# Kernel tuning notes

Hardware: AMD Instinct MI355X
Metric: run time of the kernel (lower is better)

The kernel has to match this reference:

```python
import jax, jax.numpy as jnp
import numpy as np


def conv(x, w, b=None, stride=1, pad=0):
    out = jax.lax.conv_general_dilated(x, w, (stride, stride), [(pad, pad), (pad, pad)],
                                       dimension_numbers=('NCHW', 'OIHW', 'NCHW'))
    if b is not None:
        out = out + b[None, :, None, None]
    return out


def fsm(x, att_w, conv_w):
    # FeatureSelectionModule: global-avg-pool -> 1x1 conv -> sigmoid gate, residual, 1x1 proj
    gap = jnp.mean(x, axis=(2, 3), keepdims=True)
    atten = jax.nn.sigmoid(conv(gap, att_w))
    return conv(x + x * atten, conv_w)


def mdcn(x, offset, mask, weight, bias, pad=1, G=8):
    # Modulated deformable conv v2: stride 1, dilation 1, conv groups 1, G deformable groups.
    N, C, H, W = x.shape
    Co, Ci, kh, kw = weight.shape
    K = kh * kw
    Cg = C // G
    off = offset.reshape(N, G, 2, K, H, W)          # per-group (y, x) offsets per kernel tap
    msk = mask.reshape(N, G, 1, K, H, W)
    ky, kx = jnp.meshgrid(jnp.arange(kh), jnp.arange(kw), indexing='ij')
    py = (jnp.arange(H, dtype=x.dtype)[None, None, None, :, None] - pad) + ky.reshape(1, 1, K, 1, 1) + off[:, :, 0]
    px = (jnp.arange(W, dtype=x.dtype)[None, None, None, None, :] - pad) + kx.reshape(1, 1, K, 1, 1) + off[:, :, 1]
    y0 = jnp.floor(py)
    x0 = jnp.floor(px)
    wy1 = py - y0
    wy0 = 1.0 - wy1
    wx1 = px - x0
    wx0 = 1.0 - wx1
    xg = x.reshape(N, G, Cg, H * W)

    def gather(iy, ix):
        valid = (iy >= 0) & (iy <= H - 1) & (ix >= 0) & (ix <= W - 1)
        idx = (jnp.clip(iy, 0, H - 1) * W + jnp.clip(ix, 0, W - 1)).astype(jnp.int32)
        v = jnp.take_along_axis(xg, idx.reshape(N, G, 1, K * H * W), axis=3)
        return v.reshape(N, G, Cg, K, H, W) * valid[:, :, None].astype(x.dtype)

    val = ((wy0 * wx0)[:, :, None] * gather(y0, x0)
         + (wy0 * wx1)[:, :, None] * gather(y0, x0 + 1)
         + (wy1 * wx0)[:, :, None] * gather(y0 + 1, x0)
         + (wy1 * wx1)[:, :, None] * gather(y0 + 1, x0 + 1))
    val = val * msk                                   # [N,G,Cg,K,H,W]
    out = jnp.einsum('ngckhw,ogck->nohw', val, weight.reshape(Co, G, Cg, K))
    return out + bias[None, :, None, None]


def align(feat_l, feat_s, att_w, fsm_w, off_w, om_w, om_b, dcn_w, dcn_b):
    # FeatureAlign_V2
    N, Cs, H, W = feat_s.shape[0], feat_s.shape[1], feat_l.shape[2], feat_l.shape[3]
    feat_up = jax.image.resize(feat_s, (N, Cs, H, W), 'bilinear')  # align_corners=False
    feat_arm = fsm(feat_l, att_w, fsm_w)
    off_feat = conv(jnp.concatenate([feat_arm, feat_up * 2.0], axis=1), off_w)
    om = conv(off_feat, om_w, om_b, pad=1)            # conv_offset_mask: 3*G*K channels
    o1, o2, mk = jnp.split(om, 3, axis=1)
    offset = jnp.concatenate([o1, o2], axis=1)
    mask = jax.nn.sigmoid(mk)
    feat_align = jax.nn.relu(mdcn(feat_up, offset, mask, dcn_w, dcn_b))
    return feat_align + feat_arm


def setup_inputs() -> dict:
    key = jax.random.key(0)
    ks = iter(jax.random.split(key, 64))

    def w(shape):
        fan_in = shape[1] * shape[2] * shape[3]
        return jax.random.normal(next(ks), shape, jnp.float32) / np.float32(np.sqrt(fan_in))

    def b(n):
        return jnp.zeros((n,), jnp.float32)

    d = {}
    d['c2'] = jax.random.normal(next(ks), (1, 256, 128, 128), jnp.float32)
    d['c3'] = jax.random.normal(next(ks), (1, 512, 64, 64), jnp.float32)
    d['c4'] = jax.random.normal(next(ks), (1, 1024, 32, 32), jnp.float32)
    d['c5'] = jax.random.normal(next(ks), (1, 2048, 16, 16), jnp.float32)
    OC = 256
    OM = 8 * 3 * 9  # deformable_groups * (2 offsets + 1 mask) * k*k = 216
    for tag, in_nc in (('16', 1024), ('8', 512), ('4', 256)):
        d['att_w' + tag] = w((in_nc, in_nc, 1, 1))
        d['fsm_w' + tag] = w((OC, in_nc, 1, 1))
        d['off_w' + tag] = w((OC, 2 * OC, 1, 1))
        d['om_w' + tag] = w((OM, OC, 3, 3))
        d['om_b' + tag] = b(OM)
        d['dcn_w' + tag] = w((OC, OC, 3, 3))
        d['dcn_b' + tag] = b(OC)
        d['out_w' + tag] = w((OC, OC, 3, 3))
        d['out_b' + tag] = b(OC)
    d['lat_w'] = w((OC, 2048, 1, 1))
    d['lat_b'] = b(OC)
    return d


def reference(c2, c3, c4, c5,
              att_w16, fsm_w16, off_w16, om_w16, om_b16, dcn_w16, dcn_b16, out_w16, out_b16,
              att_w8, fsm_w8, off_w8, om_w8, om_b8, dcn_w8, dcn_b8, out_w8, out_b8,
              att_w4, fsm_w4, off_w4, om_w4, om_b4, dcn_w4, dcn_b4, out_w4, out_b4,
              lat_w, lat_b):
    # top-down pass, coarsest first (matches FAN.forward with reversed inputs)
    p5 = conv(c5, lat_w, lat_b)
    f16 = align(c4, p5, att_w16, fsm_w16, off_w16, om_w16, om_b16, dcn_w16, dcn_b16)
    p4 = conv(f16, out_w16, out_b16, pad=1)
    f8 = align(c3, f16, att_w8, fsm_w8, off_w8, om_w8, om_b8, dcn_w8, dcn_b8)
    p3 = conv(f8, out_w8, out_b8, pad=1)
    f4 = align(c2, f8, att_w4, fsm_w4, off_w4, om_w4, om_b4, dcn_w4, dcn_b4)
    p2 = conv(f4, out_w4, out_b4, pad=1)
    return (p2, p3, p4, p5)
```

## Files before the change

kernel.cpp:

```cpp
#include <hip/hip_runtime.h>
#include <hip/hip_bf16.h>

typedef __hip_bfloat16 bf16;
typedef __attribute__((ext_vector_type(8))) short bf16x8;
typedef __attribute__((ext_vector_type(4))) float floatx4;

__device__ __forceinline__ float b2f(bf16 v) { return __bfloat162float(v); }
__device__ __forceinline__ bf16 f2b(float v) { return __float2bfloat16(v); }
__device__ __forceinline__ float us2f(unsigned short u) {
  union { unsigned int i; float f; } v; v.i = ((unsigned int)u) << 16; return v.f;
}
__device__ __forceinline__ unsigned short f2us(float f) {
  bf16 h = f2b(f); return *(unsigned short*)&h;
}

__global__ __launch_bounds__(256) void gap_kernel(const float* __restrict__ x,
                                                  float* __restrict__ gap,
                                                  int HW, float inv) {
  int c = blockIdx.x;
  const float* p = x + (size_t)c * HW;
  float s = 0.f;
  for (int i = threadIdx.x; i < HW; i += 256) s += p[i];
  __shared__ float red[256];
  red[threadIdx.x] = s;
  __syncthreads();
  for (int w = 128; w > 0; w >>= 1) {
    if (threadIdx.x < w) red[threadIdx.x] += red[threadIdx.x + w];
    __syncthreads();
  }
  if (threadIdx.x == 0) gap[c] = red[0] * inv;
}

__global__ __launch_bounds__(256) void atten_kernel(const float* __restrict__ w,
                                                    const float* __restrict__ gap,
                                                    float* __restrict__ scale, int Ci) {
  int wave = threadIdx.x >> 6, lane = threadIdx.x & 63;
  int o = blockIdx.x * 4 + wave;
  const float4* wr = (const float4*)(w + (size_t)o * Ci);
  const float4* g4 = (const float4*)gap;
  int n4 = Ci >> 2;
  float s = 0.f;
  for (int i = lane; i < n4; i += 64) {
    float4 a = wr[i], b = g4[i];
    s += a.x * b.x + a.y * b.y + a.z * b.z + a.w * b.w;
  }
#pragma unroll
  for (int off = 32; off > 0; off >>= 1) s += __shfl_down(s, off);
  if (lane == 0) scale[o] = 1.f + 1.f / (1.f + expf(-s));
}

__global__ __launch_bounds__(256) void upsample2x_nhwc_kernel(
    const bf16* __restrict__ src, bf16* __restrict__ dst, int Hs, int Ws) {
  int p = blockIdx.x;
  int c = threadIdx.x;
  int W = Ws * 2;
  int y = p / W, x = p - y * W;
  float fy = y * 0.5f - 0.25f;
  float fx = x * 0.5f - 0.25f;
  int y0 = (int)floorf(fy), x0 = (int)floorf(fx);
  float wy1 = fy - (float)y0, wx1 = fx - (float)x0;
  int y0c = min(max(y0, 0), Hs - 1);
  int y1c = min(max(y0 + 1, 0), Hs - 1);
  int x0c = min(max(x0, 0), Ws - 1);
  int x1c = min(max(x0 + 1, 0), Ws - 1);
  float v00 = b2f(src[(size_t)(y0c * Ws + x0c) * 256 + c]);
  float v01 = b2f(src[(size_t)(y0c * Ws + x1c) * 256 + c]);
  float v10 = b2f(src[(size_t)(y1c * Ws + x0c) * 256 + c]);
  float v11 = b2f(src[(size_t)(y1c * Ws + x1c) * 256 + c]);
  float v = (1.f - wy1) * ((1.f - wx1) * v00 + wx1 * v01)
          + wy1 * ((1.f - wx1) * v10 + wx1 * v11);
  dst[(size_t)p * 256 + c] = f2b(v);
}

__global__ __launch_bounds__(256) void packw1_kernel(const float* __restrict__ w,
                                                     bf16* __restrict__ BP, int K) {
  int idx = blockIdx.x * 256 + threadIdx.x;
  int j = idx & 7;
  int o = (idx >> 3) & 255;
  int kc8 = idx >> 11;
  int k = kc8 * 8 + j;
  BP[idx] = f2b(w[(size_t)o * K + k]);
}

__global__ __launch_bounds__(256) void pack_level_kernel(
    const float* __restrict__ fsm_w, int Ci,
    const float* __restrict__ off_w, const float* __restrict__ om_w,
    const float* __restrict__ dcn_w, const float* __restrict__ out_w,
    bf16* __restrict__ BPfsm, bf16* __restrict__ BPoff, bf16* __restrict__ BPom,
    bf16* __restrict__ BPdcn, bf16* __restrict__ BPout) {
  int b = blockIdx.x;
  if (b < Ci) {
    int idx = b * 256 + threadIdx.x;
    int j = idx & 7, o = (idx >> 3) & 255, k = (idx >> 11) * 8 + j;
    BPfsm[idx] = f2b(fsm_w[(size_t)o * Ci + k]);
    return;
  }
  b -= Ci;
  if (b < 512) {
    int idx = b * 256 + threadIdx.x;
    int j = idx & 7, o = (idx >> 3) & 255, k = (idx >> 11) * 8 + j;
    BPoff[idx] = f2b(off_w[(size_t)o * 512 + k]);
    return;
  }
  b -= 512;
  const float* w;
  bf16* BP;
  int Co;
  if (b < 2304) { w = om_w; BP = BPom; Co = 216; }
  else if (b < 4608) {
    int idx = (b - 2304) * 256 + threadIdx.x;
    int j = idx & 7, o = (idx >> 3) & 255;
    int k = (idx >> 11) * 8 + j;
    int tap = k >> 8, ci = k & 255;
    BPdcn[idx] = f2b(dcn_w[((size_t)o * 256 + ci) * 9 + tap]);
    return;
  } else { w = out_w; BP = BPout; Co = 256; b -= 2304; }
  int idx = (b % 2304) * 256 + threadIdx.x;
  int j = idx & 7;
  int t1 = idx >> 3;
  int o = t1 & 255;
  int t2 = t1 >> 8;
  int q = t2 & 3;
  int t3 = t2 >> 2;
  int tap = t3 % 9;
  int c = t3 / 9;
  int ci = c * 32 + q * 8 + j;
  float v = (o < Co) ? w[((size_t)o * 256 + ci) * 9 + tap] : 0.f;
  BP[idx] = f2b(v);
}

template <bool NCHW1, typename TA1>
__global__ __launch_bounds__(256) void conv1x1_mfma_kernel(
    const TA1* __restrict__ A1, const float* __restrict__ scaleA,
    const bf16* __restrict__ A2, float scaleB,
    int Ci1, int Ci2, int HW,
    const bf16* __restrict__ BP, const float* __restrict__ bias,
    float* __restrict__ out1, bf16* __restrict__ out2, int ns2) {
  __shared__ __align__(16) bf16 sA[1024];
  int p0 = blockIdx.x * 32;
  int tid = threadIdx.x;
  int pix = tid & 31, sub = tid >> 5;
  int pix2 = tid >> 3, sub8 = tid & 7;
  int lane = tid & 63, wave = tid >> 6;
  int pg = wave & 1, cg = wave >> 1;
  int q = lane >> 4, n = lane & 15;

  floatx4 acc[4];
#pragma unroll
  for (int nt = 0; nt < 4; ++nt) acc[nt] = (floatx4)0.f;

  int nch = (Ci1 + Ci2) >> 5;
  for (int kc = 0; kc < nch; ++kc) {
    int ci0 = kc << 5;
    if (NCHW1 && ci0 < Ci1) {
#pragma unroll
      for (int it = 0; it < 4; ++it) {
        int cil = it * 8 + sub;
        float x = (float)A1[(size_t)(ci0 + cil) * HW + p0 + pix];
        if (scaleA) x *= scaleA[ci0 + cil];
        sA[((cil >> 3) * 32 + pix) * 8 + (cil & 7)] = f2b(x);
      }
    } else {
      const bf16* src; int cb; bool scl;
      if (!NCHW1 && ci0 < Ci1) {
        src = (const bf16*)(const void*)A1; cb = ci0; scl = false;
      } else {
        src = A2; cb = ci0 - Ci1; scl = true;
      }
      ushort4 raw = *(const ushort4*)&src[(size_t)(p0 + pix2) * 256 + cb + sub8 * 4];
      if (scl) {
        raw.x = f2us(us2f(raw.x) * scaleB);
        raw.y = f2us(us2f(raw.y) * scaleB);
        raw.z = f2us(us2f(raw.z) * scaleB);
        raw.w = f2us(us2f(raw.w) * scaleB);
      }
      *(ushort4*)&sA[((sub8 >> 1) * 32 + pix2) * 8 + (sub8 & 1) * 4] = raw;
    }
    __syncthreads();
    bf16x8 a = *(const bf16x8*)&sA[(q * 32 + pg * 16 + n) * 8];
    const bf16* bp = BP + ((size_t)(kc * 4 + q) * 256 + blockIdx.y * 128 + cg * 64) * 8;
#pragma unroll
    for (int nt = 0; nt < 4; ++nt) {
      bf16x8 b = *(const bf16x8*)&bp[(nt * 16 + n) * 8];
      acc[nt] = __builtin_amdgcn_mfma_f32_16x16x32_bf16(a, b, acc[nt], 0, 0, 0);
    }
    __syncthreads();
  }

  int pbase = p0 + pg * 16 + q * 4;
#pragma unroll
  for (int nt = 0; nt < 4; ++nt) {
    int o = blockIdx.y * 128 + cg * 64 + nt * 16 + n;
    float bv = bias ? bias[o] : 0.f;
#pragma unroll
    for (int r = 0; r < 4; ++r) {
      float v = acc[nt][r] + bv;
      if (out1) out1[(size_t)o * HW + pbase + r] = v;
      if (out2) out2[(size_t)(pbase + r) * ns2 + o] = f2b(v);
    }
  }
}

__global__ __launch_bounds__(256) void conv1x1_part_kernel(
    const float* __restrict__ A1, int HW,
    const bf16* __restrict__ BP, float* __restrict__ PART) {
  __shared__ __align__(16) bf16 sA[1024];
  int p0 = blockIdx.x * 32;
  int tid = threadIdx.x;
  int pix = tid & 31, sub = tid >> 5;
  int lane = tid & 63, wave = tid >> 6;
  int pg = wave & 1, cg = wave >> 1;
  int q = lane >> 4, n = lane & 15;

  floatx4 acc[4];
#pragma unroll
  for (int nt = 0; nt < 4; ++nt) acc[nt] = (floatx4)0.f;

  int kc0 = blockIdx.z * 8;
  for (int kcl = 0; kcl < 8; ++kcl) {
    int kc = kc0 + kcl;
    int ci0 = kc << 5;
#pragma unroll
    for (int it = 0; it < 4; ++it) {
      int cil = it * 8 + sub;
      sA[((cil >> 3) * 32 + pix) * 8 + (cil & 7)] =
          f2b(A1[(size_t)(ci0 + cil) * HW + p0 + pix]);
    }
    __syncthreads();
    bf16x8 a = *(const bf16x8*)&sA[(q * 32 + pg * 16 + n) * 8];
    const bf16* bp = BP + ((size_t)(kc * 4 + q) * 256 + blockIdx.y * 128 + cg * 64) * 8;
#pragma unroll
    for (int nt = 0; nt < 4; ++nt) {
      bf16x8 b = *(const bf16x8*)&bp[(nt * 16 + n) * 8];
      acc[nt] = __builtin_amdgcn_mfma_f32_16x16x32_bf16(a, b, acc[nt], 0, 0, 0);
    }
    __syncthreads();
  }

  int pbase = p0 + pg * 16 + q * 4;
#pragma unroll
  for (int nt = 0; nt < 4; ++nt) {
    int o = blockIdx.y * 128 + cg * 64 + nt * 16 + n;
#pragma unroll
    for (int r = 0; r < 4; ++r)
      PART[((size_t)blockIdx.z * 256 + o) * HW + pbase + r] = acc[nt][r];
  }
}

__global__ __launch_bounds__(256) void reduce_p5_kernel(
    const float* __restrict__ PART, const float* __restrict__ bias,
    float* __restrict__ out1, bf16* __restrict__ out2, int HW, int KS) {
  int o = blockIdx.x;
  int p = threadIdx.x;
  float s = bias[o];
  for (int z = 0; z < KS; ++z) s += PART[((size_t)z * 256 + o) * HW + p];
  out1[(size_t)o * HW + p] = s;
  out2[(size_t)p * 256 + o] = f2b(s);
}

template <int S>
__global__ __launch_bounds__(256) void conv3x3v2_kernel(
    const bf16* __restrict__ in, const bf16* __restrict__ BP,
    const float* __restrict__ bias,
    int H, int W, int Co,
    float* __restrict__ out1, bf16* __restrict__ out2, int ns2) {
  constexpr int P = 32 * S + 2;
  constexpr int TASKS = 3 * P * 8;
  constexpr int ITS = (TASKS + 255) / 256;
  __shared__ __align__(16) bf16 sA[2][4 * 3 * P * 8];
  int HW = H * W;
  int segs = W / (32 * S);
  int y = blockIdx.x / segs;
  int x0 = (blockIdx.x - y * segs) * (32 * S);
  int tid = threadIdx.x;
  int lane = tid & 63, wave = tid >> 6;
  int pg = wave & 1, cg = wave >> 1;
  int q = lane >> 4, n = lane & 15;

  int dstIdx[ITS], srcOff[ITS];
  bool act[ITS], val[ITS];
#pragma unroll
  for (int it = 0; it < ITS; ++it) {
    int tt = it * 256 + tid;
    act[it] = (tt < TASKS);
    int sub8 = tt & 7;
    int rp = tt >> 3;
    int row = rp / P;
    int pxl = rp - row * P;
    int yy = y + row - 1;
    int xg = x0 + pxl - 1;
    bool v = act[it] && ((unsigned)yy < (unsigned)H) && ((unsigned)xg < (unsigned)W);
    val[it] = v;
    srcOff[it] = v ? ((yy * W + xg) * 256 + sub8 * 4) : 0;
    dstIdx[it] = (((sub8 >> 1) * 3 + row) * P + pxl) * 8 + (sub8 & 1) * 4;
  }

  ushort4 pv[ITS];
  auto load_regs = [&](int kc) {
    int cb = kc << 5;
#pragma unroll
    for (int it = 0; it < ITS; ++it) {
      ushort4 z = {0, 0, 0, 0};
      pv[it] = val[it] ? *(const ushort4*)&in[(size_t)srcOff[it] + cb] : z;
    }
  };
  auto store_lds = [&](int buf) {
#pragma unroll
    for (int it = 0; it < ITS; ++it)
      if (act[it]) *(ushort4*)&sA[buf][dstIdx[it]] = pv[it];
  };

  floatx4 acc[S][4];
#pragma unroll
  for (int s = 0; s < S; ++s)
#pragma unroll
    for (int nt = 0; nt < 4; ++nt) acc[s][nt] = (floatx4)0.f;

  load_regs(0);
  store_lds(0);
  __syncthreads();
  load_regs(1);

  for (int kc = 0; kc < 8; ++kc) {
    const bf16* sv = &sA[kc & 1][0];
    const bf16* bpc = BP + (size_t)kc * 73728;
#pragma unroll
    for (int tap = 0; tap < 9; ++tap) {
      int ty = tap / 3, tx = tap % 3;
      bf16x8 a[S];
#pragma unroll
      for (int s = 0; s < S; ++s)
        a[s] = *(const bf16x8*)&sv[((q * 3 + ty) * P + tx + s * 32 + pg * 16 + n) * 8];
      const bf16* bp = bpc + ((size_t)(tap * 4 + q) * 256 + blockIdx.y * 128 + cg * 64) * 8;
#pragma unroll
      for (int nt = 0; nt < 4; ++nt) {
        bf16x8 b = *(const bf16x8*)&bp[(nt * 16 + n) * 8];
#pragma unroll
        for (int s = 0; s < S; ++s)
          acc[s][nt] = __builtin_amdgcn_mfma_f32_16x16x32_bf16(a[s], b, acc[s][nt], 0, 0, 0);
      }
    }
    if (kc < 7) {
      store_lds((kc + 1) & 1);
      __syncthreads();
      if (kc < 6) load_regs(kc + 2);
    }
  }

#pragma unroll
  for (int s = 0; s < S; ++s) {
    int pbase = y * W + x0 + s * 32 + pg * 16 + q * 4;
#pragma unroll
    for (int nt = 0; nt < 4; ++nt) {
      int o = blockIdx.y * 128 + cg * 64 + nt * 16 + n;
      if (o < Co) {
        float bv = bias ? bias[o] : 0.f;
#pragma unroll
        for (int r = 0; r < 4; ++r) {
          float v = acc[s][nt][r] + bv;
          if (out1) out1[(size_t)o * HW + pbase + r] = v;
          if (out2) out2[(size_t)(pbase + r) * ns2 + o] = f2b(v);
        }
      }
    }
  }
}

__global__ __launch_bounds__(512, 4) void mdcn_mfma_kernel(
    const bf16* __restrict__ UPn, const bf16* __restrict__ OM,
    const bf16* __restrict__ BP, const float* __restrict__ dcn_b,
    const bf16* __restrict__ ARM, bf16* __restrict__ F,
    int H, int W, int wshift) {
  __shared__ __align__(16) bf16 sval[2][32 * 272];
  __shared__ float4 mw[2304];
  __shared__ int mi[2304];
  int pb = blockIdx.x * 32;
  int tid = threadIdx.x;

  for (int t2 = tid; t2 < 2304; t2 += 512) {
    int px_ = t2 & 31, g = (t2 >> 5) & 7, tap = t2 >> 8;
    int ky = tap / 3, kx = tap - ky * 3;
    int p = pb + px_;
    int y = p >> wshift, x = p & (W - 1);
    const bf16* omp = OM + (size_t)p * 216;
    float dy = b2f(omp[g * 18 + tap]);
    float dx = b2f(omp[g * 18 + 9 + tap]);
    float mm = 1.f / (1.f + expf(-b2f(omp[144 + g * 9 + tap])));
    float fpy = (float)(y - 1 + ky) + dy;
    float fpx = (float)(x - 1 + kx) + dx;
    fpy = fminf(fmaxf(fpy, -1.0e4f), 1.0e4f);
    fpx = fminf(fmaxf(fpx, -1.0e4f), 1.0e4f);
    float fy0 = floorf(fpy), fx0 = floorf(fpx);
    float wy1 = fpy - fy0, wx1 = fpx - fx0;
    float wy0 = 1.f - wy1, wx0 = 1.f - wx1;
    int iy0 = (int)fy0, ix0 = (int)fx0;
    bool vy0 = (unsigned)iy0 < (unsigned)H;
    bool vy1 = (unsigned)(iy0 + 1) < (unsigned)H;
    bool vx0 = (unsigned)ix0 < (unsigned)W;
    bool vx1 = (unsigned)(ix0 + 1) < (unsigned)W;
    float w00 = (vy0 && vx0) ? mm * wy0 * wx0 : 0.f;
    float w01 = (vy0 && vx1) ? mm * wy0 * wx1 : 0.f;
    float w10 = (vy1 && vx0) ? mm * wy1 * wx0 : 0.f;
    float w11 = (vy1 && vx1) ? mm * wy1 * wx1 : 0.f;
    int iy0c = min(max(iy0, 0), H - 1);
    int iy1c = min(max(iy0 + 1, 0), H - 1);
    int ix0c = min(max(ix0, 0), W - 1);
    int ix1c = min(max(ix0 + 1, 0), W - 1);
    mw[t2] = make_float4(w00, w01, w10, w11);
    mi[t2] = (iy0c * W + ix0c) | ((ix1c - ix0c) << 20) | ((iy1c - iy0c) << 21);
  }
  __syncthreads();

  int l4 = tid & 7;
  int px = (tid >> 3) & 31;
  int gh = tid >> 8;
  int lane = tid & 63, wave = tid >> 6;
  int q = lane >> 4, n = lane & 15;
  int rowb = l4 >> 1;
  int woff = px * 8 + (l4 & 1) * 4;

  floatx4 acc[2][2];
#pragma unroll
  for (int m = 0; m < 2; ++m)
#pragma unroll
    for (int nt = 0; nt < 2; ++nt) acc[m][nt] = (floatx4)0.f;

  ushort4 gl[4][4];
  auto gatherLoad = [&](int t) {
    int base = t * 256 + px + gh * 128;
#pragma unroll
    for (int gg = 0; gg < 4; ++gg) {
      int g = gh * 4 + gg;
      int mv = mi[base + gg * 32];
      int idx = mv & 0x3FFFF;
      int dxs = (mv >> 20) & 1;
      int dyW = ((mv >> 21) & 1) * W;
      const bf16* up = UPn + (size_t)idx * 256 + g * 32 + l4 * 4;
      gl[gg][0] = *(const ushort4*)(up);
      gl[gg][1] = *(const ushort4*)(up + dxs * 256);
      gl[gg][2] = *(const ushort4*)(up + dyW * 256);
      gl[gg][3] = *(const ushort4*)(up + (dyW + dxs) * 256);
    }
  };
  auto gatherStore = [&](int t) {
    bf16* sv = &sval[t & 1][0];
    int base = t * 256 + px + gh * 128;
#pragma unroll
    for (int gg = 0; gg < 4; ++gg) {
      int g = gh * 4 + gg;
      float4 wv = mw[base + gg * 32];
      ushort4 u00 = gl[gg][0], u01 = gl[gg][1], u10 = gl[gg][2], u11 = gl[gg][3];
      ushort4 o4;
      o4.x = f2us(wv.x * us2f(u00.x) + wv.y * us2f(u01.x)
                + wv.z * us2f(u10.x) + wv.w * us2f(u11.x));
      o4.y = f2us(wv.x * us2f(u00.y) + wv.y * us2f(u01.y)
                + wv.z * us2f(u10.y) + wv.w * us2f(u11.y));
      o4.z = f2us(wv.x * us2f(u00.z) + wv.y * us2f(u01.z)
                + wv.z * us2f(u10.z) + wv.w * us2f(u11.z));
      o4.w = f2us(wv.x * us2f(u00.w) + wv.y * us2f(u01.w)
                + wv.z * us2f(u10.w) + wv.w * us2f(u11.w));
      *(ushort4*)&sv[(g * 4 + rowb) * 272 + woff] = o4;
    }
  };

  gatherLoad(0);
  gatherStore(0);
  for (int t = 0; t < 9; ++t) {
    __syncthreads();
    if (t < 8) gatherLoad(t + 1);
    const bf16* sv = &sval[t & 1][0];
    const bf16* bpt = BP + ((size_t)(t * 32) * 256 + wave * 32) * 8;
#pragma unroll
    for (int kc = 0; kc < 8; ++kc) {
      int R = kc * 4 + q;
      bf16x8 a0 = *(const bf16x8*)&sv[R * 272 + n * 8];
      bf16x8 a1 = *(const bf16x8*)&sv[R * 272 + (16 + n) * 8];
      const bf16* bp = bpt + (size_t)R * 2048;
      bf16x8 b0 = *(const bf16x8*)&bp[n * 8];
      bf16x8 b1 = *(const bf16x8*)&bp[(16 + n) * 8];
      acc[0][0] = __builtin_amdgcn_mfma_f32_16x16x32_bf16(a0, b0, acc[0][0], 0, 0, 0);
      acc[0][1] = __builtin_amdgcn_mfma_f32_16x16x32_bf16(a0, b1, acc[0][1], 0, 0, 0);
      acc[1][0] = __builtin_amdgcn_mfma_f32_16x16x32_bf16(a1, b0, acc[1][0], 0, 0, 0);
      acc[1][1] = __builtin_amdgcn_mfma_f32_16x16x32_bf16(a1, b1, acc[1][1], 0, 0, 0);
    }
    if (t < 8) gatherStore(t + 1);
  }

#pragma unroll
  for (int m = 0; m < 2; ++m) {
#pragma unroll
    for (int nt = 0; nt < 2; ++nt) {
      int o = wave * 32 + nt * 16 + n;
      float bv = dcn_b[o];
#pragma unroll
      for (int r = 0; r < 4; ++r) {
        int p = pb + m * 16 + q * 4 + r;
        float v = fmaxf(acc[m][nt][r] + bv, 0.f) + b2f(ARM[(size_t)p * 256 + o]);
        F[(size_t)p * 256 + o] = f2b(v);
      }
    }
  }
}

extern "C" void kernel_launch(void* const* d_in, const int* in_sizes, int n_in,
                              void* d_out, int out_size, void* d_ws, size_t ws_size,
                              hipStream_t stream) {
  const float* c2 = (const float*)d_in[0];
  const float* c3 = (const float*)d_in[1];
  const float* c4 = (const float*)d_in[2];
  const float* c5 = (const float*)d_in[3];
  const float* lat_w = (const float*)d_in[31];
  const float* lat_b = (const float*)d_in[32];
  float* out = (float*)d_out;
  (void)ws_size; (void)in_sizes; (void)n_in; (void)out_size;

  const size_t p2_off = 0;
  const size_t p3_off = 4194304;
  const size_t p4_off = p3_off + 1048576;
  const size_t p5_off = p4_off + 262144;

  char* ws = (char*)d_ws;
  bf16* UPn = (bf16*)(ws);
  bf16* ARM = (bf16*)(ws + 8388608);
  bf16* FB  = (bf16*)(ws + 16777216);
  bf16* P5N = (bf16*)(ws + 25165824);
  bf16* BPout = (bf16*)(ws + 25296896);
  bf16* BPfsm = (bf16*)(ws + 26476544);
  bf16* BPoff = (bf16*)(ws + 27000832);
  float* GAP = (float*)(ws + 27262976);
  float* SC  = (float*)(ws + 27271168);
  bf16* OM = (bf16*)(out + p2_off);
  bf16* BPom = (bf16*)((char*)(out + p2_off) + 10485760);
  bf16* BPdcn = (bf16*)((char*)(out + p2_off) + 11665408);
  float* PART = (float*)ws;

  packw1_kernel<<<2048, 256, 0, stream>>>(lat_w, BPout, 2048);
  conv1x1_part_kernel<<<dim3(8, 2, 8), 256, 0, stream>>>(c5, 256, BPout, PART);
  reduce_p5_kernel<<<256, 256, 0, stream>>>(PART, lat_b, out + p5_off, P5N, 256, 8);

  struct Lv {
    const float* featl; int Ci; int H; int W; int wshift;
    float* pdst; int wbase;
  };
  Lv levels[3] = {
      {c4, 1024, 32, 32, 5, out + p4_off, 4},
      {c3, 512, 64, 64, 6, out + p3_off, 13},
      {c2, 256, 128, 128, 7, out + p2_off, 22},
  };

  for (int li = 0; li < 3; ++li) {
    const Lv& L = levels[li];
    const float* att_w = (const float*)d_in[L.wbase + 0];
    const float* fsm_w = (const float*)d_in[L.wbase + 1];
    const float* off_w = (const float*)d_in[L.wbase + 2];
    const float* om_w  = (const float*)d_in[L.wbase + 3];
    const float* om_b  = (const float*)d_in[L.wbase + 4];
    const float* dcn_w = (const float*)d_in[L.wbase + 5];
    const float* dcn_b = (const float*)d_in[L.wbase + 6];
    const float* out_w = (const float*)d_in[L.wbase + 7];
    const float* out_b = (const float*)d_in[L.wbase + 8];
    int HW = L.H * L.W;

    pack_level_kernel<<<L.Ci + 512 + 3 * 2304, 256, 0, stream>>>(
        fsm_w, L.Ci, off_w, om_w, dcn_w, out_w,
        BPfsm, BPoff, BPom, BPdcn, BPout);
    upsample2x_nhwc_kernel<<<HW, 256, 0, stream>>>(
        (li == 0) ? P5N : FB, UPn, L.H / 2, L.W / 2);
    gap_kernel<<<L.Ci, 256, 0, stream>>>(L.featl, GAP, HW, 1.f / (float)HW);
    atten_kernel<<<L.Ci / 4, 256, 0, stream>>>(att_w, GAP, SC, L.Ci);
    conv1x1_mfma_kernel<true, float><<<dim3(HW / 32, 2), 256, 0, stream>>>(
        L.featl, SC, nullptr, 0.f, L.Ci, 0, HW, BPfsm, nullptr,
        nullptr, ARM, 256);
    conv1x1_mfma_kernel<false, bf16><<<dim3(HW / 32, 2), 256, 0, stream>>>(
        ARM, nullptr, UPn, 2.f, 256, 256, HW, BPoff, nullptr,
        nullptr, FB, 256);
    if (li == 2)
      conv3x3v2_kernel<2><<<dim3(HW / 64, 2), 256, 0, stream>>>(
          FB, BPom, om_b, L.H, L.W, 216, nullptr, OM, 216);
    else
      conv3x3v2_kernel<1><<<dim3(HW / 32, 2), 256, 0, stream>>>(
          FB, BPom, om_b, L.H, L.W, 216, nullptr, OM, 216);
    mdcn_mfma_kernel<<<HW / 32, 512, 0, stream>>>(
        UPn, OM, BPdcn, dcn_b, ARM, FB, L.H, L.W, L.wshift);
    if (li == 2)
      conv3x3v2_kernel<2><<<dim3(HW / 64, 2), 256, 0, stream>>>(
          FB, BPout, out_b, L.H, L.W, 256, L.pdst, nullptr, 256);
    else
      conv3x3v2_kernel<1><<<dim3(HW / 32, 2), 256, 0, stream>>>(
          FB, BPout, out_b, L.H, L.W, 256, L.pdst, nullptr, 256);
  }
}
```

Before: 696.4 us.

## Add 64-pixel-tile deformable conv kernel with pipelined gather for finest level

Adds a modulated deformable conv kernel that processes 64 pixels per block instead of 32, so each loaded weight fragment feeds four MFMA row tiles, and uses it only for the largest pyramid level. Per-tap bilinear metadata and gathered samples are double-buffered in shared memory. Global gathers for the next tap are issued before the MFMA loop on the current tap to overlap memory latency with compute. The larger tile uses more shared memory and registers, allows one block per CU, and halves the block count.

```diff
diff --git a/kernel.cpp b/kernel.cpp
--- a/kernel.cpp
+++ b/kernel.cpp
@@ -502,6 +502,146 @@
   }
 }
 
+__global__ __launch_bounds__(512, 1) void mdcn64_mfma_kernel(
+    const bf16* __restrict__ UPn, const bf16* __restrict__ OM,
+    const bf16* __restrict__ BP, const float* __restrict__ dcn_b,
+    const bf16* __restrict__ ARM, bf16* __restrict__ F,
+    int H, int W, int wshift) {
+  __shared__ __align__(16) bf16 sval[2][32 * 520];
+  __shared__ float4 mw2[2][512];
+  __shared__ int mi2[2][512];
+  int pb = blockIdx.x * 64;
+  int tid = threadIdx.x;
+  int l4 = tid & 7;
+  int px = tid >> 3;
+  int gm = tid >> 6;
+  int pxm = tid & 63;
+  int lane = tid & 63, wave = tid >> 6;
+  int q = lane >> 4, n = lane & 15;
+  int rowb = l4 >> 1;
+  int woff = px * 8 + (l4 & 1) * 4;
+
+  int pM = pb + pxm;
+  int yM = pM >> wshift, xM = pM & (W - 1);
+  const bf16* ompM = OM + (size_t)pM * 216 + gm * 18;
+  const bf16* ommM = OM + (size_t)pM * 216 + 144 + gm * 9;
+  int slot = gm * 64 + pxm;
+
+  auto metaCompute = [&](int t, int buf) {
+    int ky = t / 3, kx = t - ky * 3;
+    float dy = b2f(ompM[t]);
+    float dx = b2f(ompM[9 + t]);
+    float mm = 1.f / (1.f + expf(-b2f(ommM[t])));
+    float fpy = (float)(yM - 1 + ky) + dy;
+    float fpx = (float)(xM - 1 + kx) + dx;
+    fpy = fminf(fmaxf(fpy, -1.0e4f), 1.0e4f);
+    fpx = fminf(fmaxf(fpx, -1.0e4f), 1.0e4f);
+    float fy0 = floorf(fpy), fx0 = floorf(fpx);
+    float wy1 = fpy - fy0, wx1 = fpx - fx0;
+    float wy0 = 1.f - wy1, wx0 = 1.f - wx1;
+    int iy0 = (int)fy0, ix0 = (int)fx0;
+    bool vy0 = (unsigned)iy0 < (unsigned)H;
+    bool vy1 = (unsigned)(iy0 + 1) < (unsigned)H;
+    bool vx0 = (unsigned)ix0 < (unsigned)W;
+    bool vx1 = (unsigned)(ix0 + 1) < (unsigned)W;
+    float w00 = (vy0 && vx0) ? mm * wy0 * wx0 : 0.f;
+    float w01 = (vy0 && vx1) ? mm * wy0 * wx1 : 0.f;
+    float w10 = (vy1 && vx0) ? mm * wy1 * wx0 : 0.f;
+    float w11 = (vy1 && vx1) ? mm * wy1 * wx1 : 0.f;
+    int iy0c = min(max(iy0, 0), H - 1);
+    int iy1c = min(max(iy0 + 1, 0), H - 1);
+    int ix0c = min(max(ix0, 0), W - 1);
+    int ix1c = min(max(ix0 + 1, 0), W - 1);
+    mw2[buf][slot] = make_float4(w00, w01, w10, w11);
+    mi2[buf][slot] = (iy0c * W + ix0c) | ((ix1c - ix0c) << 20) | ((iy1c - iy0c) << 21);
+  };
+
+  floatx4 acc[4][2];
+#pragma unroll
+  for (int m = 0; m < 4; ++m)
+#pragma unroll
+    for (int nt = 0; nt < 2; ++nt) acc[m][nt] = (floatx4)0.f;
+
+  ushort4 gl[8][4];
+  auto gatherLoad = [&](int t) {
+    int bufI = t & 1;
+#pragma unroll
+    for (int g = 0; g < 8; ++g) {
+      int mv = mi2[bufI][g * 64 + px];
+      int idx = mv & 0x3FFFF;
+      int dxs = (mv >> 20) & 1;
+      int dyW = ((mv >> 21) & 1) * W;
+      const bf16* up = UPn + (size_t)idx * 256 + g * 32 + l4 * 4;
+      gl[g][0] = *(const ushort4*)(up);
+      gl[g][1] = *(const ushort4*)(up + dxs * 256);
+      gl[g][2] = *(const ushort4*)(up + dyW * 256);
+      gl[g][3] = *(const ushort4*)(up + (dyW + dxs) * 256);
+    }
+  };
+  auto gatherStore = [&](int t) {
+    bf16* sv = &sval[t & 1][0];
+    int bufI = t & 1;
+#pragma unroll
+    for (int g = 0; g < 8; ++g) {
+      float4 wv = mw2[bufI][g * 64 + px];
+      ushort4 u00 = gl[g][0], u01 = gl[g][1], u10 = gl[g][2], u11 = gl[g][3];
+      ushort4 o4;
+      o4.x = f2us(wv.x * us2f(u00.x) + wv.y * us2f(u01.x)
+                + wv.z * us2f(u10.x) + wv.w * us2f(u11.x));
+      o4.y = f2us(wv.x * us2f(u00.y) + wv.y * us2f(u01.y)
+                + wv.z * us2f(u10.y) + wv.w * us2f(u11.y));
+      o4.z = f2us(wv.x * us2f(u00.z) + wv.y * us2f(u01.z)
+                + wv.z * us2f(u10.z) + wv.w * us2f(u11.z));
+      o4.w = f2us(wv.x * us2f(u00.w) + wv.y * us2f(u01.w)
+                + wv.z * us2f(u10.w) + wv.w * us2f(u11.w));
+      *(ushort4*)&sv[(g * 4 + rowb) * 520 + woff] = o4;
+    }
+  };
+
+  metaCompute(0, 0);
+  metaCompute(1, 1);
+  __syncthreads();
+  gatherLoad(0);
+  gatherStore(0);
+
+  for (int t = 0; t < 9; ++t) {
+    __syncthreads();
+    if (t < 8) gatherLoad(t + 1);
+    if (t < 7) metaCompute(t + 2, t & 1);
+    const bf16* sv = &sval[t & 1][0];
+    const bf16* bpt = BP + ((size_t)(t * 32) * 256 + wave * 32) * 8;
+#pragma unroll
+    for (int kc = 0; kc < 8; ++kc) {
+      int R = kc * 4 + q;
+      const bf16* bp = bpt + (size_t)R * 2048;
+      bf16x8 b0 = *(const bf16x8*)&bp[n * 8];
+      bf16x8 b1 = *(const bf16x8*)&bp[(16 + n) * 8];
+#pragma unroll
+      for (int m = 0; m < 4; ++m) {
+        bf16x8 a = *(const bf16x8*)&sv[R * 520 + (m * 16 + n) * 8];
+        acc[m][0] = __builtin_amdgcn_mfma_f32_16x16x32_bf16(a, b0, acc[m][0], 0, 0, 0);
+        acc[m][1] = __builtin_amdgcn_mfma_f32_16x16x32_bf16(a, b1, acc[m][1], 0, 0, 0);
+      }
+    }
+    if (t < 8) gatherStore(t + 1);
+  }
+
+#pragma unroll
+  for (int m = 0; m < 4; ++m) {
+#pragma unroll
+    for (int nt = 0; nt < 2; ++nt) {
+      int o = wave * 32 + nt * 16 + n;
+      float bv = dcn_b[o];
+#pragma unroll
+      for (int r = 0; r < 4; ++r) {
+        int p = pb + m * 16 + q * 4 + r;
+        float v = fmaxf(acc[m][nt][r] + bv, 0.f) + b2f(ARM[(size_t)p * 256 + o]);
+        F[(size_t)p * 256 + o] = f2b(v);
+      }
+    }
+  }
+}
+
 extern "C" void kernel_launch(void* const* d_in, const int* in_sizes, int n_in,
                               void* d_out, int out_size, void* d_ws, size_t ws_size,
                               hipStream_t stream) {
@@ -580,8 +720,12 @@
     else
       conv3x3v2_kernel<1><<<dim3(HW / 32, 2), 256, 0, stream>>>(
           FB, BPom, om_b, L.H, L.W, 216, nullptr, OM, 216);
-    mdcn_mfma_kernel<<<HW / 32, 512, 0, stream>>>(
-        UPn, OM, BPdcn, dcn_b, ARM, FB, L.H, L.W, L.wshift);
+    if (li == 2)
+      mdcn64_mfma_kernel<<<HW / 64, 512, 0, stream>>>(
+          UPn, OM, BPdcn, dcn_b, ARM, FB, L.H, L.W, L.wshift);
+    else
+      mdcn_mfma_kernel<<<HW / 32, 512, 0, stream>>>(
+          UPn, OM, BPdcn, dcn_b, ARM, FB, L.H, L.W, L.wshift);
     if (li == 2)
       conv3x3v2_kernel<2><<<dim3(HW / 64, 2), 256, 0, stream>>>(
           FB, BPout, out_b, L.H, L.W, 256, L.pdst, nullptr, 256);
```

After: 694.7 us. Within noise of the previous version (-0.2%).
